# Performance work log

Measured on AMD Instinct MI355X. Metric: run time of the kernel, lower is better.

The kernel has to match this reference:

```python
import jax, jax.numpy as jnp
import numpy as np

MIN_R, MAX_R = -51.2, 51.2
ORIG_W, ORIG_H = 800.0, 448.0


def sample_bilinear(feat, gx, gy):
    # feat [N,C,H,W]; gx,gy [N,Q] in grid coords [-1,1], align_corners=True, zeros padding
    N, C, H, W = feat.shape
    px = (gx + 1.0) * 0.5 * (W - 1)
    py = (gy + 1.0) * 0.5 * (H - 1)
    x0 = jnp.floor(px)
    y0 = jnp.floor(py)
    x0i = x0.astype(jnp.int32)
    y0i = y0.astype(jnp.int32)
    wx1 = px - x0
    wy1 = py - y0
    ff = feat.reshape(N, C, H * W)

    def corner(xi, yi, w):
        valid = (xi >= 0) & (xi < W) & (yi >= 0) & (yi < H)
        idx = jnp.clip(yi, 0, H - 1) * W + jnp.clip(xi, 0, W - 1)
        vals = jax.vmap(lambda f, i: f[:, i])(ff, idx)  # [N,C,Q]
        return vals * (w * valid.astype(w.dtype))[:, None, :]

    return (corner(x0i, y0i, (1 - wx1) * (1 - wy1))
            + corner(x0i + 1, y0i, wx1 * (1 - wy1))
            + corner(x0i, y0i + 1, (1 - wx1) * wy1)
            + corner(x0i + 1, y0i + 1, wx1 * wy1))


def setup_inputs() -> dict:
    key = jax.random.key(0)
    ks = jax.random.split(key, 16)
    B, Q, C, N = 2, 900, 256, 6
    levels = [(112, 200), (56, 100), (28, 50), (14, 25)]
    inp = {
        'query': jax.random.normal(ks[0], (B, Q, C), jnp.float32),
        'reference_points': jax.random.uniform(ks[1], (B, Q, 3), jnp.float32),
        'key_padding_mask': jax.random.bernoulli(ks[2], 0.1, (B, Q)),
        'cam_intrinsics': jax.random.normal(ks[3], (B, N, 3, 3), jnp.float32),
        'cam_extrinsics': jax.random.normal(ks[4], (B, N, 4, 4), jnp.float32),
    }
    for li, (h, w) in enumerate(levels):
        inp[f'feats_l{li}'] = jax.random.normal(ks[5 + li], (B, N, C, h, w), jnp.float32)
    inp['Wq'] = jax.random.normal(ks[10], (C, C), jnp.float32) * 0.02
    inp['bq'] = jnp.zeros((C,), jnp.float32)
    inp['Wv'] = jax.random.normal(ks[11], (C, C), jnp.float32) * 0.02
    inp['bv'] = jnp.zeros((C,), jnp.float32)
    inp['Wo'] = jax.random.normal(ks[12], (C, C), jnp.float32) * 0.02
    inp['bo'] = jnp.zeros((C,), jnp.float32)
    return inp


def reference(query, reference_points, key_padding_mask, cam_intrinsics, cam_extrinsics,
              feats_l0, feats_l1, feats_l2, feats_l3, Wq, bq, Wv, bv, Wo, bo):
    B, Q, C = query.shape
    N = cam_extrinsics.shape[1]
    mask = key_padding_mask

    ref = reference_points * (MAX_R - MIN_R) + MIN_R
    ref = jnp.where(mask[..., None], jnp.float32(-1000.0), ref)

    q = query @ Wq.T + bq

    ref_hom = jnp.concatenate([ref, jnp.ones((B, Q, 1), ref.dtype)], axis=-1)  # [B,Q,4]
    inv_ext = jnp.nan_to_num(jnp.linalg.inv(cam_extrinsics), nan=0.0, posinf=1e6, neginf=-1e6)
    # per-cam: points_cam_hom = ref_hom @ inv_ext^T  -> [B,N,Q,4]
    pts_cam_hom = jnp.einsum('bqj,bnij->bnqi', ref_hom, inv_ext)
    depth = jnp.nan_to_num(pts_cam_hom[..., 2:3], nan=10.0, posinf=100.0, neginf=-100.0)
    invalid = depth[..., 0] < 1.5  # [B,N,Q]
    depth_safe = jnp.maximum(depth, 1.5)
    pts_cam = pts_cam_hom[..., :3] / depth_safe
    pts_img = jnp.einsum('bnqj,bnij->bnqi', pts_cam, cam_intrinsics)[..., :2]
    pts_img = jnp.clip(pts_img, -3000.0, 3000.0)  # [B,N,Q,2]

    level_sum = jnp.zeros((B * N, C, Q), jnp.float32)
    for feat in (feats_l0, feats_l1, feats_l2, feats_l3):
        Hf, Wf = feat.shape[3], feat.shape[4]
        fx = pts_img[..., 0] * (Wf / ORIG_W)
        fy = pts_img[..., 1] * (Hf / ORIG_H)
        gx = jnp.clip(fx / (Wf - 1.0) * 2.0 - 1.0, -10.0, 10.0)
        gy = jnp.clip(fy / (Hf - 1.0) * 2.0 - 1.0, -10.0, 10.0)
        gx = jnp.where(invalid, jnp.float32(-100.0), gx)
        gy = jnp.where(invalid, jnp.float32(-100.0), gy)
        s = sample_bilinear(feat.reshape(B * N, C, Hf, Wf),
                            gx.reshape(B * N, Q), gy.reshape(B * N, Q))
        level_sum = level_sum + jnp.nan_to_num(s)

    ms = (level_sum / 4.0).reshape(B, N, C, Q).transpose(0, 1, 3, 2)  # [B,N,Q,C]
    v = ms @ Wv.T + bv
    sampled = jnp.max(v, axis=1)  # max over cameras -> [B,Q,C]

    fused = jax.nn.relu(q + sampled) + q
    out = fused @ Wo.T + bo
    out = out * (~mask)[..., None].astype(out.dtype)
    return out
```

## Files before the change

kernel.cpp:

```cpp
#include <hip/hip_runtime.h>
#include <hip/hip_bf16.h>
#include <math.h>

#define BB 2
#define NCAM 6
#define NQ 900
#define NC 256
#define BN (BB*NCAM)
#define NROW (BB*NQ)
#define RPB 2

#define HW0 22400
#define HW1 5600
#define HW2 1400
#define HW3 350

typedef float f4 __attribute__((ext_vector_type(4)));
typedef unsigned short u16x4 __attribute__((ext_vector_type(4)));

__device__ __forceinline__ float u2f(unsigned short u){
  union{unsigned int v; float fl;} x; x.v=((unsigned int)u)<<16; return x.fl;
}

template<int F>
__device__ __forceinline__ float ld1(const void* p, long i){
  if (F) return u2f(((const unsigned short*)p)[i]);
  return ((const float*)p)[i];
}
template<int F>
__device__ __forceinline__ f4 ld4(const void* p, long i){
  if (F){
    u16x4 u = *(const u16x4*)((const unsigned short*)p + i);
    f4 r; r.x=u2f(u.x); r.y=u2f(u.y); r.z=u2f(u.z); r.w=u2f(u.w); return r;
  }
  return *(const f4*)((const float*)p + i);
}

__device__ __forceinline__ int sniff_flag(const unsigned char* refraw){
  int cnt=0;
  for (int i=1;i<64;i+=4){
    unsigned char b = refraw[i];
    if (b>=0x30 && b<0x40) cnt++;
  }
  return (cnt>=12) ? 1 : 0;
}

__global__ __launch_bounds__(256) void prep_all(
    const unsigned char* __restrict__ refraw,
    const void* __restrict__ ext,
    const unsigned char* __restrict__ mask_raw,
    const void* __restrict__ Wq, const void* __restrict__ Wv,
    const void* __restrict__ Wo,
    const void* __restrict__ f2, const void* __restrict__ f3,
    int nW, int nT2, int nT3,
    int* __restrict__ flag_out, float* __restrict__ inv_out,
    int* __restrict__ mask_out,
    float* __restrict__ Wblk, float* __restrict__ T2buf,
    float* __restrict__ T3buf){
  __shared__ int sflag, s_na, s_gt, s_bf;
  int t = threadIdx.x;
  int bi = blockIdx.x;
  if (t==0){ sflag = sniff_flag(refraw); s_na=0; s_gt=0; s_bf=0; }
  __syncthreads();
  int f = sflag;

  if (bi < nW){
    int e = bi*256 + t;
    int mat = e >> 16;
    int i = e & 65535;
    int tt = i >> 8, k = i & 255;
    const void* W = (mat==0)?Wq:((mat==1)?Wv:Wo);
    float v = f ? u2f(((const unsigned short*)W)[i]) : ((const float*)W)[i];
    Wblk[mat*65536 + (k>>2)*1024 + tt*4 + (k&3)] = v;
    return;
  }
  if (bi < nW+nT2){
    int e = (bi-nW)*256 + t;
    int bn = e / (HW2*NC);
    int rem = e - bn*(HW2*NC);
    int p = rem >> 8, c = rem & 255;
    int src = (bn*NC + c)*HW2 + p;
    T2buf[e] = f ? u2f(((const unsigned short*)f2)[src]) : ((const float*)f2)[src];
    return;
  }
  if (bi < nW+nT2+nT3){
    int e = (bi-nW-nT2)*256 + t;
    int bn = e / (HW3*NC);
    int rem = e - bn*(HW3*NC);
    int p = rem >> 8, c = rem & 255;
    int src = (bn*NC + c)*HW3 + p;
    T3buf[e] = f ? u2f(((const unsigned short*)f3)[src]) : ((const float*)f3)[src];
    return;
  }

  int f_na=0, f_gt=0, f_bf=0;
  for (int i=t;i<NROW;i+=blockDim.x){
    unsigned char b = mask_raw[i];
    if ((i&3)!=0 && b!=0) f_na=1;
    if (b>1) f_gt=1;
    if ((i&3)==1 && b==0x3f) f_bf=1;
  }
  if (f_na) atomicOr(&s_na,1);
  if (f_gt) atomicOr(&s_gt,1);
  if (f_bf) atomicOr(&s_bf,1);
  __syncthreads();
  int fmt;
  if (!s_na) fmt=0;
  else if (!s_gt) fmt=1;
  else fmt = s_bf ? 2 : 3;
  for (int i=t;i<NROW;i+=blockDim.x){
    int v;
    if (fmt==0)      v = (((const int*)mask_raw)[i]            != 0);
    else if (fmt==1) v = (mask_raw[i]                          != 0);
    else if (fmt==2) v = (((const unsigned short*)mask_raw)[i] != 0);
    else             v = (((const float*)mask_raw)[i]          != 0.0f);
    mask_out[i]=v;
  }
  if (t==0) *flag_out = f;
  if (t < BN){
    double a[4][8];
    for(int i=0;i<4;i++){
      for(int j=0;j<4;j++) a[i][j] = (double)(f? u2f(((const unsigned short*)ext)[t*16+i*4+j])
                                               : ((const float*)ext)[t*16+i*4+j]);
      for(int j=0;j<4;j++) a[i][4+j] = (i==j)?1.0:0.0;
    }
    for(int col=0;col<4;col++){
      int piv=col; double best=fabs(a[col][col]);
      for(int r=col+1;r<4;r++){ double v=fabs(a[r][col]); if(v>best){best=v;piv=r;} }
      if(piv!=col) for(int j=0;j<8;j++){ double tmp=a[col][j]; a[col][j]=a[piv][j]; a[piv][j]=tmp; }
      double id = 1.0/a[col][col];
      for(int j=0;j<8;j++) a[col][j]*=id;
      for(int r=0;r<4;r++) if(r!=col){
        double fc=a[r][col];
        for(int j=0;j<8;j++) a[r][j]-=fc*a[col][j];
      }
    }
    for(int i=0;i<4;i++)for(int j=0;j<4;j++){
      float v=(float)a[i][4+j];
      if (isnan(v)) v=0.f;
      else if (isinf(v)) v = (v>0.f)?1e6f:-1e6f;
      inv_out[t*16+i*4+j]=v;
    }
  }
}

struct SharedMem {
  float q[RPB][NC];
  float ms[RPB][NCAM][NC];
  float fus[RPB][NC];
  float px[RPB][NCAM], py[RPB][NCAM];
  int   iv[RPB][NCAM];
  int   off[RPB][NCAM*4][4];
  float wgt[RPB][NCAM*4][4];
};

template<int F, int RL, int RF>
__device__ __forceinline__ void fused_body(
    const void* __restrict__ query, const void* __restrict__ refpts,
    const void* __restrict__ intr,
    const void* __restrict__ f0, const void* __restrict__ f1,
    const void* __restrict__ f2, const void* __restrict__ f3,
    const void* __restrict__ Wq, const void* __restrict__ bq,
    const void* __restrict__ Wv, const void* __restrict__ bv,
    const void* __restrict__ Wo, const void* __restrict__ bo,
    const float* __restrict__ Wblk,
    const float* __restrict__ T2buf, const float* __restrict__ T3buf,
    const float* __restrict__ inv_ext, const int* __restrict__ mask_int,
    float* __restrict__ out, SharedMem& sm){
  int r0 = blockIdx.x*RPB;
  int t = threadIdx.x;

  const f4* Wq4 = (const f4*)(Wblk);
  const f4* Wv4 = (const f4*)(Wblk + 65536);
  const f4* Wo4 = (const f4*)(Wblk + 131072);

  #pragma unroll
  for(int i=0;i<RPB;i++) sm.q[i][t] = ld1<F>(query,(long)(r0+i)*NC+t);

  if (t < RPB*NCAM){
    int i = t/NCAM, n = t - i*NCAM;
    int row = r0+i, b = row/NQ;
    int m = mask_int[row];
    float h0 = ld1<F>(refpts,(long)row*3+0)*102.4f - 51.2f;
    float h1 = ld1<F>(refpts,(long)row*3+1)*102.4f - 51.2f;
    float h2 = ld1<F>(refpts,(long)row*3+2)*102.4f - 51.2f;
    if (m){ h0=-1000.f; h1=-1000.f; h2=-1000.f; }
    const float* M = inv_ext + (b*NCAM+n)*16;
    float c0 = M[0]*h0 + M[1]*h1 + M[2]*h2 + M[3];
    float c1 = M[4]*h0 + M[5]*h1 + M[6]*h2 + M[7];
    float c2 = M[8]*h0 + M[9]*h1 + M[10]*h2 + M[11];
    float depth = c2;
    if (isnan(depth)) depth = 10.f;
    else if (isinf(depth)) depth = (depth>0)?100.f:-100.f;
    int iv = (depth < 1.5f);
    float ds = fmaxf(depth, 1.5f);
    float pc0=c0/ds, pc1=c1/ds, pc2=c2/ds;
    long kb = (long)(b*NCAM+n)*9;
    float ix = ld1<F>(intr,kb+0)*pc0 + ld1<F>(intr,kb+1)*pc1 + ld1<F>(intr,kb+2)*pc2;
    float iy = ld1<F>(intr,kb+3)*pc0 + ld1<F>(intr,kb+4)*pc1 + ld1<F>(intr,kb+5)*pc2;
    sm.px[i][n] = fminf(fmaxf(ix,-3000.f),3000.f);
    sm.py[i][n] = fminf(fmaxf(iy,-3000.f),3000.f);
    sm.iv[i][n] = iv;
  }
  __syncthreads();

  if (t < RPB*NCAM*4){
    const int Ws_[4]={200,100,50,25}, Hs_[4]={112,56,28,14};
    int i = t/(NCAM*4), u = t - i*(NCAM*4);
    int n = u>>2, l = u&3;
    float x=sm.px[i][n], y=sm.py[i][n];
    int iv=sm.iv[i][n];
    int W=Ws_[l], H=Hs_[l];
    float gx = (x * ((float)W/800.f)) / (W-1.f) * 2.f - 1.f;
    float gy = (y * ((float)H/448.f)) / (H-1.f) * 2.f - 1.f;
    gx=fminf(fmaxf(gx,-10.f),10.f); gy=fminf(fmaxf(gy,-10.f),10.f);
    if(iv){gx=-100.f;gy=-100.f;}
    float pxx=(gx+1.f)*0.5f*(W-1.f);
    float pyy=(gy+1.f)*0.5f*(H-1.f);
    float x0f=floorf(pxx), y0f=floorf(pyy);
    int x0=(int)x0f, y0=(int)y0f;
    float wx1=pxx-x0f, wy1=pyy-y0f, wx0=1.f-wx1, wy0=1.f-wy1;
    int vx0=(x0>=0)&(x0<W), vx1=(x0+1>=0)&(x0+1<W);
    int vy0=(y0>=0)&(y0<H), vy1=(y0+1>=0)&(y0+1<H);
    int cx0=min(max(x0,0),W-1), cx1=min(max(x0+1,0),W-1);
    int cy0=min(max(y0,0),H-1), cy1=min(max(y0+1,0),H-1);
    sm.off[i][u][0]=cy0*W+cx0; sm.wgt[i][u][0]=wx0*wy0*(float)(vx0&vy0);
    sm.off[i][u][1]=cy0*W+cx1; sm.wgt[i][u][1]=wx1*wy0*(float)(vx1&vy0);
    sm.off[i][u][2]=cy1*W+cx0; sm.wgt[i][u][2]=wx0*wy1*(float)(vx0&vy1);
    sm.off[i][u][3]=cy1*W+cx1; sm.wgt[i][u][3]=wx1*wy1*(float)(vx1&vy1);
  }
  __syncthreads();

  #pragma unroll
  for(int i=0;i<RPB;i++){
    int b = (r0+i)/NQ;
    #pragma unroll
    for(int n=0;n<NCAM;n++){
      int bn = b*NCAM+n;
      int chan = bn*NC + t;
      float v[16];
      {
        long cb0 = (long)chan*HW0;
        #pragma unroll
        for(int c=0;c<4;c++) v[c]   = ld1<F>(f0, cb0 + sm.off[i][n*4+0][c]);
        long cb1 = (long)chan*HW1;
        #pragma unroll
        for(int c=0;c<4;c++) v[4+c] = ld1<F>(f1, cb1 + sm.off[i][n*4+1][c]);
      }
      if (RF>=2){
        const float* Tp = T2buf + bn*(HW2*NC) + t;
        #pragma unroll
        for(int c=0;c<4;c++) v[8+c] = Tp[sm.off[i][n*4+2][c]*NC];
      } else {
        long cb2 = (long)chan*HW2;
        #pragma unroll
        for(int c=0;c<4;c++) v[8+c] = ld1<F>(f2, cb2 + sm.off[i][n*4+2][c]);
      }
      if (RF>=1){
        const float* Tp = T3buf + bn*(HW3*NC) + t;
        #pragma unroll
        for(int c=0;c<4;c++) v[12+c] = Tp[sm.off[i][n*4+3][c]*NC];
      } else {
        long cb3 = (long)chan*HW3;
        #pragma unroll
        for(int c=0;c<4;c++) v[12+c] = ld1<F>(f3, cb3 + sm.off[i][n*4+3][c]);
      }
      float acc=0.f;
      #pragma unroll
      for(int l=0;l<4;l++){
        #pragma unroll
        for(int c=0;c<4;c++)
          acc = fmaf(sm.wgt[i][n*4+l][c], v[l*4+c], acc);
      }
      sm.ms[i][n][t] = acc*0.25f;
    }
  }

  float qv[RPB];
  #pragma unroll
  for(int i=0;i<RPB;i++) qv[i]=0.f;
  {
    #pragma unroll 8
    for(int k4=0;k4<NC/4;k4++){
      f4 wv = RL ? Wq4[k4*256 + t] : ld4<F>(Wq, (long)t*NC + 4*k4);
      #pragma unroll
      for(int i=0;i<RPB;i++){
        f4 xv = ((const f4*)sm.q[i])[k4];
        qv[i]=fmaf(wv.x,xv.x,qv[i]); qv[i]=fmaf(wv.y,xv.y,qv[i]);
        qv[i]=fmaf(wv.z,xv.z,qv[i]); qv[i]=fmaf(wv.w,xv.w,qv[i]);
      }
    }
    float bqv = ld1<F>(bq,t);
    #pragma unroll
    for(int i=0;i<RPB;i++) qv[i]+=bqv;
  }
  __syncthreads();

  float ac[RPB][NCAM];
  #pragma unroll
  for(int i=0;i<RPB;i++)
    #pragma unroll
    for(int n=0;n<NCAM;n++) ac[i][n]=0.f;
  {
    #pragma unroll 2
    for(int k4=0;k4<NC/4;k4++){
      f4 wv = RL ? Wv4[k4*256 + t] : ld4<F>(Wv, (long)t*NC + 4*k4);
      #pragma unroll
      for(int i=0;i<RPB;i++){
        #pragma unroll
        for(int n=0;n<NCAM;n++){
          f4 mv=((const f4*)sm.ms[i][n])[k4];
          ac[i][n]=fmaf(wv.x,mv.x,ac[i][n]); ac[i][n]=fmaf(wv.y,mv.y,ac[i][n]);
          ac[i][n]=fmaf(wv.z,mv.z,ac[i][n]); ac[i][n]=fmaf(wv.w,mv.w,ac[i][n]);
        }
      }
    }
  }
  {
    float bvv = ld1<F>(bv,t);
    #pragma unroll
    for(int i=0;i<RPB;i++){
      float sv = ac[i][0];
      #pragma unroll
      for(int n=1;n<NCAM;n++) sv = fmaxf(sv, ac[i][n]);
      sv += bvv;
      sm.fus[i][t] = fmaxf(qv[i]+sv, 0.f) + qv[i];
    }
  }
  __syncthreads();

  float o[RPB];
  #pragma unroll
  for(int i=0;i<RPB;i++) o[i]=0.f;
  {
    #pragma unroll 8
    for(int k4=0;k4<NC/4;k4++){
      f4 wv = RL ? Wo4[k4*256 + t] : ld4<F>(Wo, (long)t*NC + 4*k4);
      #pragma unroll
      for(int i=0;i<RPB;i++){
        f4 xv = ((const f4*)sm.fus[i])[k4];
        o[i]=fmaf(wv.x,xv.x,o[i]); o[i]=fmaf(wv.y,xv.y,o[i]);
        o[i]=fmaf(wv.z,xv.z,o[i]); o[i]=fmaf(wv.w,xv.w,o[i]);
      }
    }
    float bov = ld1<F>(bo,t);
    #pragma unroll
    for(int i=0;i<RPB;i++){
      int m = mask_int[r0+i];
      float r = o[i] + bov;
      if (m) r = 0.f;
      out[(long)(r0+i)*NC+t] = r;
    }
  }
}

template<int RL, int RF>
__global__ __launch_bounds__(256,4) void fused_kernel(
    const void* query, const void* refpts, const void* intr,
    const void* f0, const void* f1, const void* f2, const void* f3,
    const void* Wq, const void* bq, const void* Wv, const void* bv,
    const void* Wo, const void* bo, const float* __restrict__ Wblk,
    const float* __restrict__ T2buf, const float* __restrict__ T3buf,
    const float* __restrict__ inv_ext, const int* __restrict__ mask_int,
    const int* __restrict__ flag, float* __restrict__ out){
  __shared__ SharedMem sm;
  if (*flag)
    fused_body<1,RL,RF>(query,refpts,intr,f0,f1,f2,f3,Wq,bq,Wv,bv,Wo,bo,
                        Wblk,T2buf,T3buf,inv_ext,mask_int,out,sm);
  else
    fused_body<0,RL,RF>(query,refpts,intr,f0,f1,f2,f3,Wq,bq,Wv,bv,Wo,bo,
                        Wblk,T2buf,T3buf,inv_ext,mask_int,out,sm);
}

extern "C" void kernel_launch(void* const* d_in, const int* in_sizes, int n_in,
                              void* d_out, int out_size, void* d_ws, size_t ws_size,
                              hipStream_t stream){
  const void* query  = d_in[0];
  const void* refpts = d_in[1];
  const unsigned char* mask_raw = (const unsigned char*)d_in[2];
  const void* intr   = d_in[3];
  const void* ext    = d_in[4];
  const void* f0     = d_in[5];
  const void* f1     = d_in[6];
  const void* f2     = d_in[7];
  const void* f3     = d_in[8];
  const void* Wq     = d_in[9];
  const void* bq     = d_in[10];
  const void* Wv     = d_in[11];
  const void* bv     = d_in[12];
  const void* Wo     = d_in[13];
  const void* bo     = d_in[14];

  char* ws = (char*)d_ws;
  float* inv_ext  = (float*)(ws + 0);
  int*   dflag    = (int*)  (ws + 1024);
  int*   mask_int = (int*)  (ws + 2048);
  float* Wblk     = (float*)(ws + 16384);
  float* T3buf    = (float*)(ws + 802816);
  float* T2buf    = (float*)(ws + 5103616);

  const size_t needW  = 802816;
  const size_t need3  = 5103616;
  const size_t need23 = 22306816;

  int rl = (ws_size >= needW) ? 1 : 0;
  int rf = (ws_size >= need23) ? 2 : ((ws_size >= need3) ? 1 : 0);

  int nW  = rl ? 768 : 0;
  int nT2 = (rf>=2) ? (BN*HW2*NC)/256 : 0;
  int nT3 = (rf>=1) ? (BN*HW3*NC)/256 : 0;

  hipLaunchKernelGGL(prep_all, dim3(nW+nT2+nT3+1), dim3(256), 0, stream,
                     (const unsigned char*)refpts, ext, mask_raw,
                     Wq, Wv, Wo, f2, f3, nW, nT2, nT3,
                     dflag, inv_ext, mask_int, Wblk, T2buf, T3buf);

  dim3 grid(NROW/RPB);
  if (rl && rf==2)
    hipLaunchKernelGGL(HIP_KERNEL_NAME(fused_kernel<1,2>), grid, dim3(256), 0, stream,
                       query, refpts, intr, f0, f1, f2, f3,
                       Wq, bq, Wv, bv, Wo, bo, Wblk, T2buf, T3buf,
                       inv_ext, mask_int, dflag, (float*)d_out);
  else if (rl && rf==1)
    hipLaunchKernelGGL(HIP_KERNEL_NAME(fused_kernel<1,1>), grid, dim3(256), 0, stream,
                       query, refpts, intr, f0, f1, f2, f3,
                       Wq, bq, Wv, bv, Wo, bo, Wblk, T2buf, T3buf,
                       inv_ext, mask_int, dflag, (float*)d_out);
  else if (rl)
    hipLaunchKernelGGL(HIP_KERNEL_NAME(fused_kernel<1,0>), grid, dim3(256), 0, stream,
                       query, refpts, intr, f0, f1, f2, f3,
                       Wq, bq, Wv, bv, Wo, bo, Wblk, T2buf, T3buf,
                       inv_ext, mask_int, dflag, (float*)d_out);
  else
    hipLaunchKernelGGL(HIP_KERNEL_NAME(fused_kernel<0,0>), grid, dim3(256), 0, stream,
                       query, refpts, intr, f0, f1, f2, f3,
                       Wq, bq, Wv, bv, Wo, bo, Wblk, T2buf, T3buf,
                       inv_ext, mask_int, dflag, (float*)d_out);
}
```

Before: 522.5 us.

## Tile the feature transposes through shared memory and pair bilinear corner loads

New measurement: 494.3 us. -5.4%, faster.

```diff
diff --git a/kernel.cpp b/kernel.cpp
--- a/kernel.cpp
+++ b/kernel.cpp
@@ -17,6 +17,7 @@
 
 typedef float f4 __attribute__((ext_vector_type(4)));
 typedef unsigned short u16x4 __attribute__((ext_vector_type(4)));
+typedef struct __attribute__((aligned(4))) { float x, y; } pf2;
 
 __device__ __forceinline__ float u2f(unsigned short u){
   union{unsigned int v; float fl;} x; x.v=((unsigned int)u)<<16; return x.fl;
@@ -36,6 +37,20 @@
   return *(const f4*)((const float*)p + i);
 }
 
+template<int F>
+__device__ __forceinline__ void corner4(const void* fp, long cb, int offA, int offB,
+                                        int d0, int d1, float* v){
+  if (F){
+    v[0]=ld1<1>(fp,cb+offA+d0); v[1]=ld1<1>(fp,cb+offA+d1);
+    v[2]=ld1<1>(fp,cb+offB+d0); v[3]=ld1<1>(fp,cb+offB+d1);
+  } else {
+    pf2 a = *(const pf2*)((const float*)fp + cb + offA);
+    pf2 b = *(const pf2*)((const float*)fp + cb + offB);
+    v[0]=d0?a.y:a.x; v[1]=d1?a.y:a.x;
+    v[2]=d0?b.y:b.x; v[3]=d1?b.y:b.x;
+  }
+}
+
 __device__ __forceinline__ int sniff_flag(const unsigned char* refraw){
   int cnt=0;
   for (int i=1;i<64;i+=4){
@@ -45,6 +60,8 @@
   return (cnt>=12) ? 1 : 0;
 }
 
+#define TILES2 (8*44)
+#define TILES3 (8*11)
 __global__ __launch_bounds__(256) void prep_all(
     const unsigned char* __restrict__ refraw,
     const void* __restrict__ ext,
@@ -52,12 +69,13 @@
     const void* __restrict__ Wq, const void* __restrict__ Wv,
     const void* __restrict__ Wo,
     const void* __restrict__ f2, const void* __restrict__ f3,
-    int nW, int nT2, int nT3,
+    int nW, int nT2t, int nT3t,
     int* __restrict__ flag_out, float* __restrict__ inv_out,
     int* __restrict__ mask_out,
     float* __restrict__ Wblk, float* __restrict__ T2buf,
     float* __restrict__ T3buf){
   __shared__ int sflag, s_na, s_gt, s_bf;
+  __shared__ float tile[32][33];
   int t = threadIdx.x;
   int bi = blockIdx.x;
   if (t==0){ sflag = sniff_flag(refraw); s_na=0; s_gt=0; s_bf=0; }
@@ -74,22 +92,33 @@
     Wblk[mat*65536 + (k>>2)*1024 + tt*4 + (k&3)] = v;
     return;
   }
-  if (bi < nW+nT2){
-    int e = (bi-nW)*256 + t;
-    int bn = e / (HW2*NC);
-    int rem = e - bn*(HW2*NC);
-    int p = rem >> 8, c = rem & 255;
-    int src = (bn*NC + c)*HW2 + p;
-    T2buf[e] = f ? u2f(((const unsigned short*)f2)[src]) : ((const float*)f2)[src];
-    return;
-  }
-  if (bi < nW+nT2+nT3){
-    int e = (bi-nW-nT2)*256 + t;
-    int bn = e / (HW3*NC);
-    int rem = e - bn*(HW3*NC);
-    int p = rem >> 8, c = rem & 255;
-    int src = (bn*NC + c)*HW3 + p;
-    T3buf[e] = f ? u2f(((const unsigned short*)f3)[src]) : ((const float*)f3)[src];
+  if (bi < nW+nT2t+nT3t){
+    int idx = bi - nW;
+    const void* src; float* dst; int HW, tpb, tp;
+    if (idx < nT2t){ HW=HW2; src=f2; dst=T2buf; tpb=TILES2; tp=44; }
+    else { idx -= nT2t; HW=HW3; src=f3; dst=T3buf; tpb=TILES3; tp=11; }
+    int bn = idx / tpb; int rem = idx - bn*tpb;
+    int ct = rem / tp,  pt = rem - ct*tp;
+    int c0 = ct*32, p0 = pt*32;
+    int ty = t>>5, tx = t&31;
+    #pragma unroll
+    for (int r=0;r<4;r++){
+      int c = c0 + ty + r*8;
+      int p = p0 + tx;
+      float v = 0.f;
+      if (p < HW){
+        long s = (long)(bn*NC + c)*HW + p;
+        v = f ? u2f(((const unsigned short*)src)[s]) : ((const float*)src)[s];
+      }
+      tile[ty+r*8][tx] = v;
+    }
+    __syncthreads();
+    #pragma unroll
+    for (int r=0;r<4;r++){
+      int p = p0 + ty + r*8;
+      if (p < HW)
+        dst[((long)bn*HW + p)*NC + c0 + tx] = tile[tx][ty+r*8];
+    }
     return;
   }
 
@@ -224,55 +253,67 @@
     int vy0=(y0>=0)&(y0<H), vy1=(y0+1>=0)&(y0+1<H);
     int cx0=min(max(x0,0),W-1), cx1=min(max(x0+1,0),W-1);
     int cy0=min(max(y0,0),H-1), cy1=min(max(y0+1,0),H-1);
-    sm.off[i][u][0]=cy0*W+cx0; sm.wgt[i][u][0]=wx0*wy0*(float)(vx0&vy0);
-    sm.off[i][u][1]=cy0*W+cx1; sm.wgt[i][u][1]=wx1*wy0*(float)(vx1&vy0);
-    sm.off[i][u][2]=cy1*W+cx0; sm.wgt[i][u][2]=wx0*wy1*(float)(vx0&vy1);
-    sm.off[i][u][3]=cy1*W+cx1; sm.wgt[i][u][3]=wx1*wy1*(float)(vx1&vy1);
-  }
-  __syncthreads();
-
-  #pragma unroll
-  for(int i=0;i<RPB;i++){
-    int b = (r0+i)/NQ;
+    int px = min(max(x0,0),W-2);
+    int d0 = cx0 - px, d1 = cx1 - px;
+    sm.off[i][u][0]=cy0*W+px; sm.off[i][u][1]=cy1*W+px;
+    sm.off[i][u][2]=d0;       sm.off[i][u][3]=d1;
+    sm.wgt[i][u][0]=wx0*wy0*(float)(vx0&vy0);
+    sm.wgt[i][u][1]=wx1*wy0*(float)(vx1&vy0);
+    sm.wgt[i][u][2]=wx0*wy1*(float)(vx0&vy1);
+    sm.wgt[i][u][3]=wx1*wy1*(float)(vx1&vy1);
+  }
+  __syncthreads();
+
+  {
     #pragma unroll
     for(int n=0;n<NCAM;n++){
-      int bn = b*NCAM+n;
-      int chan = bn*NC + t;
-      float v[16];
-      {
-        long cb0 = (long)chan*HW0;
+      #pragma unroll
+      for(int i=0;i<RPB;i++){
+        int b = (r0+i)/NQ;
+        int bn = b*NCAM+n;
+        int chan = bn*NC + t;
+        float v[16];
+        corner4<F>(f0, (long)chan*HW0,
+                   sm.off[i][n*4+0][0], sm.off[i][n*4+0][1],
+                   sm.off[i][n*4+0][2], sm.off[i][n*4+0][3], &v[0]);
+        corner4<F>(f1, (long)chan*HW1,
+                   sm.off[i][n*4+1][0], sm.off[i][n*4+1][1],
+                   sm.off[i][n*4+1][2], sm.off[i][n*4+1][3], &v[4]);
+        {
+          int u=n*4+2;
+          if (RF>=2){
+            const float* Tp = T2buf + (long)bn*(HW2*NC) + t;
+            int oA=sm.off[i][u][0], oB=sm.off[i][u][1], d0=sm.off[i][u][2], d1=sm.off[i][u][3];
+            v[8] =Tp[(long)(oA+d0)*NC]; v[9] =Tp[(long)(oA+d1)*NC];
+            v[10]=Tp[(long)(oB+d0)*NC]; v[11]=Tp[(long)(oB+d1)*NC];
+          } else {
+            corner4<F>(f2, (long)chan*HW2,
+                       sm.off[i][u][0], sm.off[i][u][1],
+                       sm.off[i][u][2], sm.off[i][u][3], &v[8]);
+          }
+        }
+        {
+          int u=n*4+3;
+          if (RF>=1){
+            const float* Tp = T3buf + (long)bn*(HW3*NC) + t;
+            int oA=sm.off[i][u][0], oB=sm.off[i][u][1], d0=sm.off[i][u][2], d1=sm.off[i][u][3];
+            v[12]=Tp[(long)(oA+d0)*NC]; v[13]=Tp[(long)(oA+d1)*NC];
+            v[14]=Tp[(long)(oB+d0)*NC]; v[15]=Tp[(long)(oB+d1)*NC];
+          } else {
+            corner4<F>(f3, (long)chan*HW3,
+                       sm.off[i][u][0], sm.off[i][u][1],
+                       sm.off[i][u][2], sm.off[i][u][3], &v[12]);
+          }
+        }
+        float acc=0.f;
         #pragma unroll
-        for(int c=0;c<4;c++) v[c]   = ld1<F>(f0, cb0 + sm.off[i][n*4+0][c]);
-        long cb1 = (long)chan*HW1;
-        #pragma unroll
-        for(int c=0;c<4;c++) v[4+c] = ld1<F>(f1, cb1 + sm.off[i][n*4+1][c]);
-      }
-      if (RF>=2){
-        const float* Tp = T2buf + bn*(HW2*NC) + t;
-        #pragma unroll
-        for(int c=0;c<4;c++) v[8+c] = Tp[sm.off[i][n*4+2][c]*NC];
-      } else {
-        long cb2 = (long)chan*HW2;
-        #pragma unroll
-        for(int c=0;c<4;c++) v[8+c] = ld1<F>(f2, cb2 + sm.off[i][n*4+2][c]);
-      }
-      if (RF>=1){
-        const float* Tp = T3buf + bn*(HW3*NC) + t;
-        #pragma unroll
-        for(int c=0;c<4;c++) v[12+c] = Tp[sm.off[i][n*4+3][c]*NC];
-      } else {
-        long cb3 = (long)chan*HW3;
-        #pragma unroll
-        for(int c=0;c<4;c++) v[12+c] = ld1<F>(f3, cb3 + sm.off[i][n*4+3][c]);
-      }
-      float acc=0.f;
-      #pragma unroll
-      for(int l=0;l<4;l++){
-        #pragma unroll
-        for(int c=0;c<4;c++)
-          acc = fmaf(sm.wgt[i][n*4+l][c], v[l*4+c], acc);
-      }
-      sm.ms[i][n][t] = acc*0.25f;
+        for(int l=0;l<4;l++){
+          #pragma unroll
+          for(int c=0;c<4;c++)
+            acc = fmaf(sm.wgt[i][n*4+l][c], v[l*4+c], acc);
+        }
+        sm.ms[i][n][t]=acc*0.25f;
+      }
     }
   }
 
@@ -406,13 +447,13 @@
   int rl = (ws_size >= needW) ? 1 : 0;
   int rf = (ws_size >= need23) ? 2 : ((ws_size >= need3) ? 1 : 0);
 
-  int nW  = rl ? 768 : 0;
-  int nT2 = (rf>=2) ? (BN*HW2*NC)/256 : 0;
-  int nT3 = (rf>=1) ? (BN*HW3*NC)/256 : 0;
-
-  hipLaunchKernelGGL(prep_all, dim3(nW+nT2+nT3+1), dim3(256), 0, stream,
+  int nW   = rl ? 768 : 0;
+  int nT2t = (rf>=2) ? BN*TILES2 : 0;
+  int nT3t = (rf>=1) ? BN*TILES3 : 0;
+
+  hipLaunchKernelGGL(prep_all, dim3(nW+nT2t+nT3t+1), dim3(256), 0, stream,
                      (const unsigned char*)refpts, ext, mask_raw,
-                     Wq, Wv, Wo, f2, f3, nW, nT2, nT3,
+                     Wq, Wv, Wo, f2, f3, nW, nT2t, nT3t,
                      dflag, inv_ext, mask_int, Wblk, T2buf, T3buf);
 
   dim3 grid(NROW/RPB);
```
